# Optimization experiments

Measured on AMD Instinct MI355X. Metric: run time of the kernel, lower is better.

Reference implementation:

```python
import jax, jax.numpy as jnp
import numpy as np

B, T, D, E, F = 4, 2048, 1024, 8, 1024

def setup_inputs() -> dict:
    key = jax.random.key(0)
    ks = jax.random.split(key, 5)
    s = lambda d: 1.0 / np.sqrt(d)
    return {
        "x": jax.random.normal(ks[0], (B, T, D), dtype=jnp.float32),
        "router_kernel_DE": jax.random.normal(ks[1], (D, E), dtype=jnp.float32) * s(D),
        "kernel_gating_EDF": jax.random.normal(ks[2], (E, D, F), dtype=jnp.float32) * s(D),
        "kernel_up_EDF": jax.random.normal(ks[3], (E, D, F), dtype=jnp.float32) * s(D),
        "kernel_down_EFD": jax.random.normal(ks[4], (E, F, D), dtype=jnp.float32) * s(F),
        "top_k": 2,
    }

def reference(x, router_kernel_DE, kernel_gating_EDF, kernel_up_EDF, kernel_down_EFD, top_k):
    # ---- Router ----
    router_logits_BTE = jnp.einsum('BTD,DE->BTE', x, router_kernel_DE)
    probs_BTE = jax.nn.softmax(router_logits_BTE.astype(jnp.float32), axis=-1)
    weights_BTX, selected_BTX = jax.lax.top_k(probs_BTE, top_k)
    # module re-normalizes top-k weights with a second softmax (faithful)
    norm_weights_BTX = jax.nn.softmax(weights_BTX, axis=-1)
    # ---- combine weights to dense per-expert weights ----
    one_hot_BTXE = jax.nn.one_hot(selected_BTX, num_classes=E, dtype=jnp.float32)
    full_weights_BTE = jnp.sum(one_hot_BTXE * norm_weights_BTX[..., None], axis=2)
    # ---- dense all-experts MLP (apply_expert_weight_before_computation=False) ----
    gating_BTEF = jnp.einsum('BTD,EDF->BTEF', x, kernel_gating_EDF)
    up_BTEF = jnp.einsum('BTD,EDF->BTEF', x, kernel_up_EDF)
    fuse_BTEF = jax.nn.silu(gating_BTEF) * up_BTEF
    down_BTED = jnp.einsum('BTEF,EFD->BTED', fuse_BTEF, kernel_down_EFD)
    out_BTD = jnp.einsum('BTED,BTE->BTD', down_BTED, full_weights_BTE)
    return out_BTD
```

## Files before the change

kernel.cpp:

```cpp
#include <hip/hip_runtime.h>
#include <hip/hip_bf16.h>
#include <math.h>

#define NTOK 8192
#define D_DIM 1024
#define E_DIM 8
#define F_DIM 1024

#define CNT_STRIDE 32

typedef __attribute__((ext_vector_type(8))) short bf16x8;
typedef __attribute__((ext_vector_type(4))) float f32x4;

typedef const __attribute__((address_space(1))) unsigned int* as1_uint_ptr;
typedef __attribute__((address_space(3))) unsigned int* as3_uint_ptr;

__device__ __forceinline__ void async_load16(const void* g, void* l) {
    __builtin_amdgcn_global_load_lds((as1_uint_ptr)g, (as3_uint_ptr)l, 16, 0, 0);
}

__device__ __forceinline__ float bf2f(unsigned short b) {
    unsigned int u = ((unsigned int)b) << 16;
    return __builtin_bit_cast(float, u);
}
__device__ __forceinline__ unsigned short f2bf(float f) {
    __hip_bfloat16 h = __float2bfloat16(f);
    return __builtin_bit_cast(unsigned short, h);
}


__global__ __launch_bounds__(512) void prep_kernel(
    const float* __restrict__ x,
    const float* __restrict__ Wr,
    int* __restrict__ cnt,
    int* __restrict__ tok_of,
    float* __restrict__ wt2,
    unsigned short* __restrict__ xb,
    const float* __restrict__ Wg, const float* __restrict__ Wu,
    const float* __restrict__ Wd,
    unsigned short* __restrict__ WgT, unsigned short* __restrict__ WuT,
    unsigned short* __restrict__ WdT)
{
    const int tid = threadIdx.x;

    if (blockIdx.x >= 256) {
        __shared__ float tile[2][64][65];
        const int s = tid >> 8;
        const int t2 = tid & 255;
        const int k = (blockIdx.x - 256) * 2 + s;
        const int m = k >> 8;
        const int rem = k & 255;
        const int c0 = (rem & 15) * 64;
        const int r0 = (rem >> 4) * 64;
        const float* src;
        unsigned short* dst;
        if (m < 8)       { src = Wg + (size_t)m * 1048576;        dst = WgT + (size_t)m * 1048576; }
        else if (m < 16) { src = Wu + (size_t)(m - 8) * 1048576;  dst = WuT + (size_t)(m - 8) * 1048576; }
        else             { src = Wd + (size_t)(m - 16) * 1048576; dst = WdT + (size_t)(m - 16) * 1048576; }

        const int tr = t2 >> 4;
        const int tc = (t2 & 15) * 4;
        #pragma unroll
        for (int p = 0; p < 4; ++p) {
            float4 v = *(const float4*)(src + (size_t)(r0 + p * 16 + tr) * 1024 + c0 + tc);
            tile[s][p * 16 + tr][tc + 0] = v.x;
            tile[s][p * 16 + tr][tc + 1] = v.y;
            tile[s][p * 16 + tr][tc + 2] = v.z;
            tile[s][p * 16 + tr][tc + 3] = v.w;
        }
        __syncthreads();
        const int orow = t2 >> 3;
        const int ocol = (t2 & 7) * 8;
        #pragma unroll
        for (int p = 0; p < 2; ++p) {
            int fr = p * 32 + orow;
            union { unsigned short us[8]; uint4 v; } pk;
            #pragma unroll
            for (int q = 0; q < 8; ++q) pk.us[q] = f2bf(tile[s][ocol + q][fr]);
            *(uint4*)&dst[(size_t)(c0 + fr) * 1024 + r0 + ocol] = pk.v;
        }
        return;
    }

    __shared__ int lcnt[E_DIM];
    __shared__ int lbase[E_DIM];
    __shared__ int lbuf[E_DIM][64];

    const int wv = tid >> 6;
    const int lane = tid & 63;
    if (tid < E_DIM) lcnt[tid] = 0;
    __syncthreads();

    #pragma unroll
    for (int it = 0; it < 4; ++it) {
        const int t = blockIdx.x * 32 + wv * 4 + it;
        const float* xrow = x + (size_t)t * D_DIM;
        unsigned short* xbrow = xb + (size_t)t * D_DIM;

        float p[E_DIM];
        #pragma unroll
        for (int e = 0; e < E_DIM; ++e) p[e] = 0.f;

        #pragma unroll
        for (int i = 0; i < 4; ++i) {
            const int d = i * 256 + lane * 4;
            float4 v = *(const float4*)(xrow + d);
            ushort4 o;
            o.x = f2bf(v.x); o.y = f2bf(v.y); o.z = f2bf(v.z); o.w = f2bf(v.w);
            *(ushort4*)(xbrow + d) = o;
            const float* wr = Wr + (size_t)d * E_DIM;
            float xv[4] = {v.x, v.y, v.z, v.w};
            #pragma unroll
            for (int q = 0; q < 4; ++q) {
                float4 w0 = *(const float4*)(wr + q * 8);
                float4 w1 = *(const float4*)(wr + q * 8 + 4);
                p[0] += xv[q] * w0.x; p[1] += xv[q] * w0.y;
                p[2] += xv[q] * w0.z; p[3] += xv[q] * w0.w;
                p[4] += xv[q] * w1.x; p[5] += xv[q] * w1.y;
                p[6] += xv[q] * w1.z; p[7] += xv[q] * w1.w;
            }
        }

        #pragma unroll
        for (int off = 32; off > 0; off >>= 1) {
            #pragma unroll
            for (int e = 0; e < E_DIM; ++e)
                p[e] += __shfl_xor(p[e], off, 64);
        }

        if (lane == 0) {
            float m = p[0];
            #pragma unroll
            for (int e = 1; e < E_DIM; ++e) m = fmaxf(m, p[e]);
            float pr[E_DIM], sum = 0.f;
            #pragma unroll
            for (int e = 0; e < E_DIM; ++e) { pr[e] = expf(p[e] - m); sum += pr[e]; }
            float inv = 1.f / sum;
            #pragma unroll
            for (int e = 0; e < E_DIM; ++e) pr[e] *= inv;
            int e0 = 0;
            #pragma unroll
            for (int e = 1; e < E_DIM; ++e) if (pr[e] > pr[e0]) e0 = e;
            int e1 = (e0 == 0) ? 1 : 0;
            #pragma unroll
            for (int e = 0; e < E_DIM; ++e) { if (e != e0 && pr[e] > pr[e1]) e1 = e; }
            float b = expf(pr[e1] - pr[e0]);
            float w0 = 1.f / (1.f + b);
            float w1 = b / (1.f + b);
            int p0 = atomicAdd(&lcnt[e0], 1);
            lbuf[e0][p0] = t * 2 + 0;
            int p1 = atomicAdd(&lcnt[e1], 1);
            lbuf[e1][p1] = t * 2 + 1;
            wt2[t * 2 + 0] = w0;
            wt2[t * 2 + 1] = w1;
        }
    }
    __syncthreads();
    if (tid < E_DIM) lbase[tid] = atomicAdd(&cnt[tid * CNT_STRIDE], lcnt[tid]);
    __syncthreads();
    #pragma unroll
    for (int e = 0; e < E_DIM; ++e) {
        int n = lcnt[e];
        if (tid < n) tok_of[e * NTOK + lbase[e] + tid] = lbuf[e][tid];
    }
}

__global__ __launch_bounds__(256, 2) void gateup_mfma(
    const unsigned short* __restrict__ xb,
    const unsigned short* __restrict__ WgT,
    const unsigned short* __restrict__ WuT,
    const int* __restrict__ cnt,
    const int* __restrict__ tok_of,
    unsigned short* __restrict__ H)
{
    const int colTile = blockIdx.x & 7;
    const int wk = blockIdx.x >> 3;
    int e = -1, rowBase = 0, rows = 0, tb = 0;
    #pragma unroll
    for (int q = 0; q < E_DIM; ++q) {
        int r = cnt[q * CNT_STRIDE];
        int nt = (r + 127) >> 7;
        if (e < 0 && wk < tb + nt) { e = q; rowBase = (wk - tb) << 7; rows = r; }
        tb += nt;
    }
    if (e < 0) return;
    const int n0 = colTile * 128;

    __shared__ short As[2][128 * 32];
    __shared__ short Bg[2][128 * 32];
    __shared__ short Bu[2][128 * 32];
    __shared__ int toks[128];

    const int tid = threadIdx.x;
    if (tid < 128) {
        int idx = rowBase + tid;
        toks[tid] = tok_of[e * NTOK + (idx < rows ? idx : rows - 1)];
    }
    __syncthreads();

    const int lane = tid & 63;
    const int w = tid >> 6;
    const int seg0 = w * 2, seg1 = w * 2 + 1;
    const int sr = lane >> 2;
    const int swz = (sr >> 1) & 3;
    const int sk = ((lane & 3) ^ swz) * 8;

    const int ar0 = seg0 * 16 + sr;
    const int ar1 = seg1 * 16 + sr;
    const unsigned short* aG0 = xb + (size_t)(toks[ar0] >> 1) * D_DIM + sk;
    const unsigned short* aG1 = xb + (size_t)(toks[ar1] >> 1) * D_DIM + sk;
    const unsigned short* WgTe = WgT + (size_t)e * F_DIM * D_DIM;
    const unsigned short* WuTe = WuT + (size_t)e * F_DIM * D_DIM;
    const unsigned short* gG0 = WgTe + (size_t)(n0 + ar0) * D_DIM + sk;
    const unsigned short* gG1 = WgTe + (size_t)(n0 + ar1) * D_DIM + sk;
    const unsigned short* uG0 = WuTe + (size_t)(n0 + ar0) * D_DIM + sk;
    const unsigned short* uG1 = WuTe + (size_t)(n0 + ar1) * D_DIM + sk;

    const int mseg = (w >> 1) * 4;
    const int nseg = (w & 1) * 4;
    const int mbase = (w >> 1) * 64;
    const int nbase = (w & 1) * 64;
    const int fr = lane & 15;
    const int rd = (4 * fr + ((lane >> 4) ^ ((fr >> 1) & 3))) * 8;

    f32x4 accg[4][4], accu[4][4];
    #pragma unroll
    for (int i = 0; i < 4; ++i)
        #pragma unroll
        for (int j = 0; j < 4; ++j) { accg[i][j] = (f32x4)(0.f); accu[i][j] = (f32x4)(0.f); }

    #define STAGE_GU(b, kk) do { \
        async_load16(aG0 + (kk), &As[b][seg0 * 512]); \
        async_load16(aG1 + (kk), &As[b][seg1 * 512]); \
        async_load16(gG0 + (kk), &Bg[b][seg0 * 512]); \
        async_load16(gG1 + (kk), &Bg[b][seg1 * 512]); \
        async_load16(uG0 + (kk), &Bu[b][seg0 * 512]); \
        async_load16(uG1 + (kk), &Bu[b][seg1 * 512]); \
    } while (0)

    const int NT = D_DIM / 32;
    STAGE_GU(0, 0);
    STAGE_GU(1, 32);

    #pragma unroll 2
    for (int t = 0; t < NT - 1; ++t) {
        const int b = t & 1;
        asm volatile("s_waitcnt vmcnt(6)" ::: "memory");
        __builtin_amdgcn_s_barrier();

        bf16x8 a[4], g[4], u[4];
        #pragma unroll
        for (int i = 0; i < 4; ++i)
            a[i] = *(const bf16x8*)&As[b][(mseg + i) * 512 + rd];
        #pragma unroll
        for (int j = 0; j < 4; ++j) {
            g[j] = *(const bf16x8*)&Bg[b][(nseg + j) * 512 + rd];
            u[j] = *(const bf16x8*)&Bu[b][(nseg + j) * 512 + rd];
        }
        asm volatile("s_waitcnt lgkmcnt(0)" ::: "memory");
        __builtin_amdgcn_sched_barrier(0);
        __builtin_amdgcn_s_barrier();
        if (t < NT - 2) STAGE_GU(b, (t + 2) * 32);

        __builtin_amdgcn_s_setprio(1);
        #pragma unroll
        for (int i = 0; i < 4; ++i)
            #pragma unroll
            for (int j = 0; j < 4; ++j) {
                accg[i][j] = __builtin_amdgcn_mfma_f32_16x16x32_bf16(a[i], g[j], accg[i][j], 0, 0, 0);
                accu[i][j] = __builtin_amdgcn_mfma_f32_16x16x32_bf16(a[i], u[j], accu[i][j], 0, 0, 0);
            }
        __builtin_amdgcn_s_setprio(0);
    }
    {
        asm volatile("s_waitcnt vmcnt(0)" ::: "memory");
        __builtin_amdgcn_s_barrier();
        bf16x8 a[4], g[4], u[4];
        #pragma unroll
        for (int i = 0; i < 4; ++i)
            a[i] = *(const bf16x8*)&As[1][(mseg + i) * 512 + rd];
        #pragma unroll
        for (int j = 0; j < 4; ++j) {
            g[j] = *(const bf16x8*)&Bg[1][(nseg + j) * 512 + rd];
            u[j] = *(const bf16x8*)&Bu[1][(nseg + j) * 512 + rd];
        }
        __builtin_amdgcn_s_setprio(1);
        #pragma unroll
        for (int i = 0; i < 4; ++i)
            #pragma unroll
            for (int j = 0; j < 4; ++j) {
                accg[i][j] = __builtin_amdgcn_mfma_f32_16x16x32_bf16(a[i], g[j], accg[i][j], 0, 0, 0);
                accu[i][j] = __builtin_amdgcn_mfma_f32_16x16x32_bf16(a[i], u[j], accu[i][j], 0, 0, 0);
            }
        __builtin_amdgcn_s_setprio(0);
    }
    #undef STAGE_GU

    const int erow = (lane >> 4) * 4;
    #pragma unroll
    for (int i = 0; i < 4; ++i) {
        #pragma unroll
        for (int r = 0; r < 4; ++r) {
            int row = mbase + i * 16 + erow + r;
            int idx = rowBase + row;
            if (idx < rows) {
                int tok2 = toks[row];
                unsigned short* hrow = H + (size_t)tok2 * F_DIM + n0 + nbase;
                #pragma unroll
                for (int j = 0; j < 4; ++j) {
                    float gg = accg[i][j][r];
                    float uu = accu[i][j][r];
                    float h = gg / (1.f + __expf(-gg)) * uu;
                    hrow[j * 16 + fr] = f2bf(h);
                }
            }
        }
    }
}

__global__ __launch_bounds__(256, 2) void down_mfma(
    const unsigned short* __restrict__ H,
    const unsigned short* __restrict__ WdT,
    const int* __restrict__ cnt,
    const int* __restrict__ tok_of,
    const float* __restrict__ wt2,
    float* __restrict__ out)
{
    const int colTile = blockIdx.x & 7;
    const int wk = blockIdx.x >> 3;
    int e = -1, rowBase = 0, rows = 0, tb = 0;
    #pragma unroll
    for (int q = 0; q < E_DIM; ++q) {
        int r = cnt[q * CNT_STRIDE];
        int nt = (r + 127) >> 7;
        if (e < 0 && wk < tb + nt) { e = q; rowBase = (wk - tb) << 7; rows = r; }
        tb += nt;
    }
    if (e < 0) return;
    const int n0 = colTile * 128;

    __shared__ short As[2][128 * 32];
    __shared__ short Bs[2][128 * 32];
    __shared__ int toks[128];

    const int tid = threadIdx.x;
    if (tid < 128) {
        int idx = rowBase + tid;
        toks[tid] = tok_of[e * NTOK + (idx < rows ? idx : rows - 1)];
    }
    __syncthreads();

    const int lane = tid & 63;
    const int w = tid >> 6;
    const int seg0 = w * 2, seg1 = w * 2 + 1;
    const int sr = lane >> 2;
    const int swz = (sr >> 1) & 3;
    const int sk = ((lane & 3) ^ swz) * 8;

    const int ar0 = seg0 * 16 + sr;
    const int ar1 = seg1 * 16 + sr;
    const unsigned short* aG0 = H + (size_t)toks[ar0] * F_DIM + sk;
    const unsigned short* aG1 = H + (size_t)toks[ar1] * F_DIM + sk;
    const unsigned short* WdTe = WdT + (size_t)e * D_DIM * F_DIM;
    const unsigned short* bG0 = WdTe + (size_t)(n0 + ar0) * F_DIM + sk;
    const unsigned short* bG1 = WdTe + (size_t)(n0 + ar1) * F_DIM + sk;

    const int mseg = (w >> 1) * 4;
    const int nseg = (w & 1) * 4;
    const int mbase = (w >> 1) * 64;
    const int nbase = (w & 1) * 64;
    const int fr = lane & 15;
    const int rd = (4 * fr + ((lane >> 4) ^ ((fr >> 1) & 3))) * 8;

    f32x4 acc[4][4];
    #pragma unroll
    for (int i = 0; i < 4; ++i)
        #pragma unroll
        for (int j = 0; j < 4; ++j) acc[i][j] = (f32x4)(0.f);

    #define STAGE_D(b, kk) do { \
        async_load16(aG0 + (kk), &As[b][seg0 * 512]); \
        async_load16(aG1 + (kk), &As[b][seg1 * 512]); \
        async_load16(bG0 + (kk), &Bs[b][seg0 * 512]); \
        async_load16(bG1 + (kk), &Bs[b][seg1 * 512]); \
    } while (0)

    const int NT = F_DIM / 32;
    STAGE_D(0, 0);
    STAGE_D(1, 32);

    #pragma unroll 2
    for (int t = 0; t < NT - 1; ++t) {
        const int b = t & 1;
        asm volatile("s_waitcnt vmcnt(4)" ::: "memory");
        __builtin_amdgcn_s_barrier();

        bf16x8 a[4], bb[4];
        #pragma unroll
        for (int i = 0; i < 4; ++i)
            a[i] = *(const bf16x8*)&As[b][(mseg + i) * 512 + rd];
        #pragma unroll
        for (int j = 0; j < 4; ++j)
            bb[j] = *(const bf16x8*)&Bs[b][(nseg + j) * 512 + rd];

        asm volatile("s_waitcnt lgkmcnt(0)" ::: "memory");
        __builtin_amdgcn_sched_barrier(0);
        __builtin_amdgcn_s_barrier();
        if (t < NT - 2) STAGE_D(b, (t + 2) * 32);

        __builtin_amdgcn_s_setprio(1);
        #pragma unroll
        for (int i = 0; i < 4; ++i)
            #pragma unroll
            for (int j = 0; j < 4; ++j)
                acc[i][j] = __builtin_amdgcn_mfma_f32_16x16x32_bf16(a[i], bb[j], acc[i][j], 0, 0, 0);
        __builtin_amdgcn_s_setprio(0);
    }
    {
        asm volatile("s_waitcnt vmcnt(0)" ::: "memory");
        __builtin_amdgcn_s_barrier();
        bf16x8 a[4], bb[4];
        #pragma unroll
        for (int i = 0; i < 4; ++i)
            a[i] = *(const bf16x8*)&As[1][(mseg + i) * 512 + rd];
        #pragma unroll
        for (int j = 0; j < 4; ++j)
            bb[j] = *(const bf16x8*)&Bs[1][(nseg + j) * 512 + rd];
        __builtin_amdgcn_s_setprio(1);
        #pragma unroll
        for (int i = 0; i < 4; ++i)
            #pragma unroll
            for (int j = 0; j < 4; ++j)
                acc[i][j] = __builtin_amdgcn_mfma_f32_16x16x32_bf16(a[i], bb[j], acc[i][j], 0, 0, 0);
        __builtin_amdgcn_s_setprio(0);
    }
    #undef STAGE_D

    const int erow = (lane >> 4) * 4;
    #pragma unroll
    for (int i = 0; i < 4; ++i) {
        #pragma unroll
        for (int r = 0; r < 4; ++r) {
            int row = mbase + i * 16 + erow + r;
            int idx = rowBase + row;
            if (idx < rows) {
                int tok2 = toks[row];
                float wgt = wt2[tok2];
                float* orow = out + (size_t)(tok2 >> 1) * D_DIM + n0 + nbase;
                #pragma unroll
                for (int j = 0; j < 4; ++j)
                    atomicAdd(&orow[j * 16 + fr], acc[i][j][r] * wgt);
            }
        }
    }
}

extern "C" void kernel_launch(void* const* d_in, const int* in_sizes, int n_in,
                              void* d_out, int out_size, void* d_ws, size_t ws_size,
                              hipStream_t stream) {
    const float* x  = (const float*)d_in[0];
    const float* Wr = (const float*)d_in[1];
    const float* Wg = (const float*)d_in[2];
    const float* Wu = (const float*)d_in[3];
    const float* Wd = (const float*)d_in[4];
    float* out = (float*)d_out;

    char* ws = (char*)d_ws;
    int*   cnt    = (int*)ws;
    int*   tok_of = (int*)(ws + 1024);
    float* wt2    = (float*)(ws + 1024 + E_DIM * NTOK * 4);
    char*  base   = ws + (1 << 20);
    unsigned short* xb  = (unsigned short*)(base);
    unsigned short* WgT = (unsigned short*)(base + (16ll << 20));
    unsigned short* WuT = (unsigned short*)(base + (32ll << 20));
    unsigned short* WdT = (unsigned short*)(base + (48ll << 20));
    unsigned short* H   = (unsigned short*)(base + (64ll << 20));

    hipMemsetAsync(cnt, 0, E_DIM * CNT_STRIDE * sizeof(int), stream);
    hipMemsetAsync(out, 0, (size_t)NTOK * D_DIM * sizeof(float), stream);

    prep_kernel<<<256 + 3072, 512, 0, stream>>>(
        x, Wr, cnt, tok_of, wt2, xb, Wg, Wu, Wd, WgT, WuT, WdT);

    const int MAX_TILES = (2 * NTOK) / 128 + E_DIM;
    gateup_mfma<<<dim3(MAX_TILES * 8), 256, 0, stream>>>(
        xb, WgT, WuT, cnt, tok_of, H);
    down_mfma<<<dim3(MAX_TILES * 8), 256, 0, stream>>>(
        H, WdT, cnt, tok_of, wt2, out);
}
```

Measured before the change: 376.6 us.

## Store expert outputs contiguously and replace atomic scatter with combine kernel

The gate/up kernel now writes H rows in expert-sorted contiguous order instead of scattering by token slot, so the down kernel reads A rows contiguously. The down kernel writes unweighted bf16 results per token slot into a buffer that reuses the xb region, and a new combine kernel forms the weighted sum of the two slots per token. This removes the output memset and the float atomicAdd traffic, at the cost of an extra kernel launch, an extra bf16 round-trip of the down results, and the precision loss from rounding them to bf16.

```diff
diff --git a/kernel.cpp b/kernel.cpp
--- a/kernel.cpp
+++ b/kernel.cpp
@@ -175,12 +175,15 @@
 {
     const int colTile = blockIdx.x & 7;
     const int wk = blockIdx.x >> 3;
-    int e = -1, rowBase = 0, rows = 0, tb = 0;
+    int e = -1, rowBase = 0, rows = 0, tb = 0, rp = 0;
     #pragma unroll
     for (int q = 0; q < E_DIM; ++q) {
         int r = cnt[q * CNT_STRIDE];
         int nt = (r + 127) >> 7;
-        if (e < 0 && wk < tb + nt) { e = q; rowBase = (wk - tb) << 7; rows = r; }
+        if (e < 0) {
+            if (wk < tb + nt) { e = q; rowBase = (wk - tb) << 7; rows = r; }
+            else rp += r;
+        }
         tb += nt;
     }
     if (e < 0) return;
@@ -304,8 +307,7 @@
             int row = mbase + i * 16 + erow + r;
             int idx = rowBase + row;
             if (idx < rows) {
-                int tok2 = toks[row];
-                unsigned short* hrow = H + (size_t)tok2 * F_DIM + n0 + nbase;
+                unsigned short* hrow = H + (size_t)(rp + idx) * F_DIM + n0 + nbase;
                 #pragma unroll
                 for (int j = 0; j < 4; ++j) {
                     float gg = accg[i][j][r];
@@ -323,17 +325,19 @@
     const unsigned short* __restrict__ WdT,
     const int* __restrict__ cnt,
     const int* __restrict__ tok_of,
-    const float* __restrict__ wt2,
-    float* __restrict__ out)
+    unsigned short* __restrict__ Hd)
 {
     const int colTile = blockIdx.x & 7;
     const int wk = blockIdx.x >> 3;
-    int e = -1, rowBase = 0, rows = 0, tb = 0;
+    int e = -1, rowBase = 0, rows = 0, tb = 0, rp = 0;
     #pragma unroll
     for (int q = 0; q < E_DIM; ++q) {
         int r = cnt[q * CNT_STRIDE];
         int nt = (r + 127) >> 7;
-        if (e < 0 && wk < tb + nt) { e = q; rowBase = (wk - tb) << 7; rows = r; }
+        if (e < 0) {
+            if (wk < tb + nt) { e = q; rowBase = (wk - tb) << 7; rows = r; }
+            else rp += r;
+        }
         tb += nt;
     }
     if (e < 0) return;
@@ -359,8 +363,10 @@
 
     const int ar0 = seg0 * 16 + sr;
     const int ar1 = seg1 * 16 + sr;
-    const unsigned short* aG0 = H + (size_t)toks[ar0] * F_DIM + sk;
-    const unsigned short* aG1 = H + (size_t)toks[ar1] * F_DIM + sk;
+    int ra0 = rowBase + ar0; if (ra0 >= rows) ra0 = rows - 1;
+    int ra1 = rowBase + ar1; if (ra1 >= rows) ra1 = rows - 1;
+    const unsigned short* aG0 = H + (size_t)(rp + ra0) * F_DIM + sk;
+    const unsigned short* aG1 = H + (size_t)(rp + ra1) * F_DIM + sk;
     const unsigned short* WdTe = WdT + (size_t)e * D_DIM * F_DIM;
     const unsigned short* bG0 = WdTe + (size_t)(n0 + ar0) * F_DIM + sk;
     const unsigned short* bG1 = WdTe + (size_t)(n0 + ar1) * F_DIM + sk;
@@ -445,14 +451,33 @@
             int idx = rowBase + row;
             if (idx < rows) {
                 int tok2 = toks[row];
-                float wgt = wt2[tok2];
-                float* orow = out + (size_t)(tok2 >> 1) * D_DIM + n0 + nbase;
+                unsigned short* orow = Hd + (size_t)tok2 * D_DIM + n0 + nbase;
                 #pragma unroll
                 for (int j = 0; j < 4; ++j)
-                    atomicAdd(&orow[j * 16 + fr], acc[i][j][r] * wgt);
+                    orow[j * 16 + fr] = f2bf(acc[i][j][r]);
             }
         }
     }
+}
+
+__global__ __launch_bounds__(256) void combine_kernel(
+    const unsigned short* __restrict__ Hd,
+    const float* __restrict__ wt2,
+    float* __restrict__ out)
+{
+    const int t = blockIdx.x;
+    const int tid = threadIdx.x;
+    const float w0 = wt2[2 * t];
+    const float w1 = wt2[2 * t + 1];
+    const int c = tid * 4;
+    ushort4 a = *(const ushort4*)&Hd[(size_t)(2 * t) * D_DIM + c];
+    ushort4 b = *(const ushort4*)&Hd[(size_t)(2 * t + 1) * D_DIM + c];
+    float4 o;
+    o.x = w0 * bf2f(a.x) + w1 * bf2f(b.x);
+    o.y = w0 * bf2f(a.y) + w1 * bf2f(b.y);
+    o.z = w0 * bf2f(a.z) + w1 * bf2f(b.z);
+    o.w = w0 * bf2f(a.w) + w1 * bf2f(b.w);
+    *(float4*)(out + (size_t)t * D_DIM + c) = o;
 }
 
 extern "C" void kernel_launch(void* const* d_in, const int* in_sizes, int n_in,
@@ -471,13 +496,13 @@
     float* wt2    = (float*)(ws + 1024 + E_DIM * NTOK * 4);
     char*  base   = ws + (1 << 20);
     unsigned short* xb  = (unsigned short*)(base);
+    unsigned short* Hd  = (unsigned short*)(base);
     unsigned short* WgT = (unsigned short*)(base + (16ll << 20));
     unsigned short* WuT = (unsigned short*)(base + (32ll << 20));
     unsigned short* WdT = (unsigned short*)(base + (48ll << 20));
     unsigned short* H   = (unsigned short*)(base + (64ll << 20));
 
     hipMemsetAsync(cnt, 0, E_DIM * CNT_STRIDE * sizeof(int), stream);
-    hipMemsetAsync(out, 0, (size_t)NTOK * D_DIM * sizeof(float), stream);
 
     prep_kernel<<<256 + 3072, 512, 0, stream>>>(
         x, Wr, cnt, tok_of, wt2, xb, Wg, Wu, Wd, WgT, WuT, WdT);
@@ -486,5 +511,6 @@
     gateup_mfma<<<dim3(MAX_TILES * 8), 256, 0, stream>>>(
         xb, WgT, WuT, cnt, tok_of, H);
     down_mfma<<<dim3(MAX_TILES * 8), 256, 0, stream>>>(
-        H, WdT, cnt, tok_of, wt2, out);
-}
+        H, WdT, cnt, tok_of, Hd);
+    combine_kernel<<<NTOK, 256, 0, stream>>>(Hd, wt2, out);
+}
```

After: 343.7 us. 1.1x faster.
